# Kernel optimization log

Hardware: AMD Instinct MI355X
Metric: run time of the kernel (lower is better)

Reference implementation:

```python
import jax, jax.numpy as jnp
import numpy as np

EPS = 1e-5


def _layernorm(h, g, b):
    mu = jnp.mean(h, axis=-1, keepdims=True)
    var = jnp.mean((h - mu) ** 2, axis=-1, keepdims=True)
    return (h - mu) * jax.lax.rsqrt(var + EPS) * g + b


def _encode(x, W1, b1, g1, be1):
    # Linear -> LayerNorm -> ReLU (Dropout is identity in eval mode)
    h = x @ W1 + b1
    return jax.nn.relu(_layernorm(h, g1, be1))


def setup_inputs() -> dict:
    key = jax.random.key(0)
    ks = jax.random.split(key, 12)
    B, N, F, H, O = 131072, 8, 9, 64, 64

    def xavier(k, shape, gain=0.5):
        fan_in, fan_out = shape[0], shape[1]
        a = gain * np.sqrt(6.0 / (fan_in + fan_out))
        return jax.random.uniform(k, shape, jnp.float32, -a, a)

    return {
        "current_node_features": jax.random.normal(ks[0], (B, F), jnp.float32),
        "neighbor_features": jax.random.normal(ks[1], (B, N, F), jnp.float32),
        "neighbor_mask": jax.random.randint(ks[2], (B, N), 0, 2, jnp.int32),
        # node_encoder
        "W_enc": xavier(ks[3], (F, H)), "b_enc": jnp.zeros((H,), jnp.float32),
        "g_enc": jnp.ones((H,), jnp.float32), "be_enc": jnp.zeros((H,), jnp.float32),
        # attention MLP
        "W_a1": xavier(ks[4], (2 * H, H)), "b_a1": jnp.zeros((H,), jnp.float32),
        "W_a2": xavier(ks[5], (H, 1)), "b_a2": jnp.zeros((1,), jnp.float32),
        # output projection
        "W_out": xavier(ks[6], (2 * H, O)), "b_out": jnp.zeros((O,), jnp.float32),
        "g_out": jnp.ones((O,), jnp.float32), "be_out": jnp.zeros((O,), jnp.float32),
    }


def reference(current_node_features, neighbor_features, neighbor_mask,
              W_enc, b_enc, g_enc, be_enc,
              W_a1, b_a1, W_a2, b_a2,
              W_out, b_out, g_out, be_out):
    B, N = neighbor_mask.shape
    cur = _encode(current_node_features, W_enc, b_enc, g_enc, be_enc)      # [B, H]
    nbr = _encode(neighbor_features, W_enc, b_enc, g_enc, be_enc)          # [B, N, H]

    cur_exp = jnp.broadcast_to(cur[:, None, :], nbr.shape)                 # [B, N, H]
    att_in = jnp.concatenate([cur_exp, nbr], axis=-1)                      # [B, N, 2H]
    scores = (jax.nn.relu(att_in @ W_a1 + b_a1) @ W_a2 + b_a2)[..., 0]     # [B, N]
    scores = jnp.where(neighbor_mask == 0, -jnp.inf, scores)
    weights = jax.nn.softmax(scores, axis=-1)
    weights = jnp.where(jnp.isnan(weights), 0.0, weights)                  # all-masked rows -> 0

    aggregated = jnp.einsum("bn,bnh->bh", weights, nbr)                    # [B, H]
    combined = jnp.concatenate([cur, aggregated], axis=-1)                 # [B, 2H]
    out = jax.nn.relu(_layernorm(combined @ W_out + b_out, g_out, be_out)) # [B, O]
    return out
```

## Files before the change

kernel.cpp:

```cpp
#include <hip/hip_runtime.h>
#include <hip/hip_bf16.h>
#include <hip/hip_fp16.h>

typedef __attribute__((ext_vector_type(8))) short bf16x8;
typedef __attribute__((ext_vector_type(4))) float f32x4;
typedef __attribute__((ext_vector_type(4))) unsigned int u32x4;
typedef __attribute__((ext_vector_type(2))) unsigned int u32x2;

#define MFMA_BF16(A,B,C) __builtin_amdgcn_mfma_f32_16x16x32_bf16((A),(B),(C),0,0,0)

static __device__ __forceinline__ unsigned int pkbf2(float a, float b) {
  __hip_bfloat162 h = __float22bfloat162_rn(make_float2(a, b));
  unsigned int u; __builtin_memcpy(&u, &h, sizeof(u));
  return u;
}
static __device__ __forceinline__ unsigned short f2bf1(float f) {
  __hip_bfloat16 h = __float2bfloat16(f);
  unsigned short u; __builtin_memcpy(&u, &h, sizeof(u));
  return u;
}
static __device__ __forceinline__ int swz8(int v) { return (v ^ (v >> 3)) & 7; }

__global__ void gcn_prep(const float* __restrict__ wa1, const float* __restrict__ wout,
                         const float* __restrict__ wenc,
                         unsigned short* __restrict__ wa1f, unsigned short* __restrict__ woutf,
                         unsigned short* __restrict__ wencT) {
  int i = blockIdx.x * 512 + threadIdx.x;
  if (i < 8192) {
    int e = i & 7, l = (i >> 3) & 63, f = i >> 9;
    int kt = f >> 2, nt = f & 3;
    int k = 32 * kt + 8 * (l >> 4) + e;
    int col = 16 * nt + (l & 15);
    wa1f[i]  = f2bf1(wa1 [k * 64 + col]);
    woutf[i] = f2bf1(wout[k * 64 + col]);
  }
  int j = i - 8192;
  if (j >= 0 && j < 2048) {
    int e = j & 7, l = (j >> 3) & 63, mt = j >> 9;
    int k = 8 * (l >> 4) + e;
    int ch = 16 * mt + (l & 15);
    wencT[j] = (k < 9) ? f2bf1(wenc[k * 64 + ch]) : (unsigned short)0;
  }
}

__global__ __launch_bounds__(128, 4) void gcn_main(
    const float* __restrict__ xcur, const float* __restrict__ xnbr,
    const int*   __restrict__ msk,
    const float* __restrict__ benc, const float* __restrict__ genc, const float* __restrict__ beenc,
    const float* __restrict__ ba1,  const float* __restrict__ wa2,
    const float* __restrict__ bout, const float* __restrict__ gout, const float* __restrict__ beout,
    const unsigned short* __restrict__ wa1f, const unsigned short* __restrict__ woutf,
    const unsigned short* __restrict__ wencT,
    float* __restrict__ out) {

  __shared__ __align__(16) char smem[20992];
  unsigned short* sE   = (unsigned short*)smem;
  unsigned short* sAgg = (unsigned short*)(smem + 18432);
  float*          sS   = (float*)(smem + 20480);
  float*          sLN  = (float*)(smem + 20480);

  const int tid  = threadIdx.x;
  const int w    = tid >> 6;
  const int lane = tid & 63;
  const int lm   = lane & 15, g = lane >> 4;
  const int blk  = blockIdx.x;

  bf16x8 wf[16];
  bf16x8 wof[8];
  float bov[2], gvo[2], bevo[2];
  int4 mkv[4];

  {
    bf16x8 ef[4];
    #pragma unroll
    for (int mt = 0; mt < 4; mt++) ef[mt] = *(const bf16x8*)(wencT + (mt * 64 + lane) * 8);
    f32x4 bv[4], gv[4], bev[4];
    #pragma unroll
    for (int mt = 0; mt < 4; mt++) {
      bv[mt]  = *(const f32x4*)(benc  + 16 * mt + 4 * g);
      gv[mt]  = *(const f32x4*)(genc  + 16 * mt + 4 * g);
      bev[mt] = *(const f32x4*)(beenc + 16 * mt + 4 * g);
    }
    float nx[8];
    {
      const float* xb = (w < 8) ? (xnbr + ((size_t)blk * 128 + w * 16 + lm) * 9)
                                : (xcur + ((size_t)blk * 16 + lm) * 9);
      #pragma unroll
      for (int e = 0; e < 8; e++) nx[e] = 0.f;
      if (g == 0) {
        #pragma unroll
        for (int e = 0; e < 8; e++) nx[e] = xb[e];
      } else if (g == 1) nx[0] = xb[8];
    }
    #pragma unroll
    for (int s5 = 0; s5 < 5; s5++) {
      int t = 2 * s5 + w;
      if (t > 8) break;
      float xv[8];
      #pragma unroll
      for (int e = 0; e < 8; e++) xv[e] = nx[e];
      int tn = t + 2;
      if (tn <= 8) {
        const float* xb = (tn < 8) ? (xnbr + ((size_t)blk * 128 + tn * 16 + lm) * 9)
                                   : (xcur + ((size_t)blk * 16 + lm) * 9);
        #pragma unroll
        for (int e = 0; e < 8; e++) nx[e] = 0.f;
        if (g == 0) {
          #pragma unroll
          for (int e = 0; e < 8; e++) nx[e] = xb[e];
        } else if (g == 1) nx[0] = xb[8];
      }
      int v = (t < 8) ? (t * 16 + lm) : (128 + lm);
      u32x4 bq;
      #pragma unroll
      for (int e2 = 0; e2 < 4; e2++) bq[e2] = pkbf2(xv[2 * e2], xv[2 * e2 + 1]);
      bf16x8 bfr = __builtin_bit_cast(bf16x8, bq);
      f32x4 acc[4];
      #pragma unroll
      for (int mt = 0; mt < 4; mt++) acc[mt] = f32x4{0.f, 0.f, 0.f, 0.f};
      #pragma unroll
      for (int mt = 0; mt < 4; mt++) acc[mt] = MFMA_BF16(ef[mt], bfr, acc[mt]);
      float hv[16]; float s1 = 0.f, s2 = 0.f;
      #pragma unroll
      for (int mt = 0; mt < 4; mt++)
        #pragma unroll
        for (int i = 0; i < 4; i++) {
          float h = acc[mt][i] + bv[mt][i];
          hv[4 * mt + i] = h; s1 += h; s2 = fmaf(h, h, s2);
        }
      s1 += __shfl_xor(s1, 16); s1 += __shfl_xor(s1, 32);
      s2 += __shfl_xor(s2, 16); s2 += __shfl_xor(s2, 32);
      float mu = s1 * (1.f / 64.f);
      float rs = rsqrtf(s2 * (1.f / 64.f) - mu * mu + 1e-5f);
      int h8 = swz8(v);
      #pragma unroll
      for (int mt = 0; mt < 4; mt++) {
        float y0 = fmaxf(fmaf((hv[4 * mt + 0] - mu) * rs, gv[mt][0], bev[mt][0]), 0.f);
        float y1 = fmaxf(fmaf((hv[4 * mt + 1] - mu) * rs, gv[mt][1], bev[mt][1]), 0.f);
        float y2 = fmaxf(fmaf((hv[4 * mt + 2] - mu) * rs, gv[mt][2], bev[mt][2]), 0.f);
        float y3 = fmaxf(fmaf((hv[4 * mt + 3] - mu) * rs, gv[mt][3], bev[mt][3]), 0.f);
        int unit = (2 * mt + (g >> 1)) ^ h8;
        *(u32x2*)&sE[v * 64 + unit * 8 + ((g & 1) << 2)] = u32x2{pkbf2(y0, y1), pkbf2(y2, y3)};
      }
    }
    #pragma unroll
    for (int f = 0; f < 16; f++) wf[f] = *(const bf16x8*)(wa1f + (f * 64 + lane) * 8);
    #pragma unroll
    for (int mm = 0; mm < 4; mm++) {
      int r2 = 8 * w + 2 * mm + (g >> 1);
      mkv[mm] = *(const int4*)(msk + ((size_t)(blk * 16 + r2)) * 8 + 4 * (g & 1));
    }
  }
  __syncthreads();

  {
    float wa2v[4], ba1v[4];
    #pragma unroll
    for (int nt = 0; nt < 4; nt++) { wa2v[nt] = wa2[16 * nt + lm]; ba1v[nt] = ba1[16 * nt + lm]; }
    #pragma unroll
    for (int mm = 0; mm < 4; mm++) {
      int m = 4 * w + mm;
      int vb = 16 * m + lm,  hb = swz8(vb);
      int vcu = 128 + 2 * m + (lm >> 3), hcu = swz8(vcu);
      f32x4 a2[4];
      #pragma unroll
      for (int nt = 0; nt < 4; nt++) a2[nt] = f32x4{0.f, 0.f, 0.f, 0.f};
      #pragma unroll
      for (int ks = 0; ks < 2; ks++) {
        bf16x8 a = *(const bf16x8*)&sE[vcu * 64 + (((4 * ks + g) ^ hcu) << 3)];
        #pragma unroll
        for (int nt = 0; nt < 4; nt++) a2[nt] = MFMA_BF16(a, wf[ks * 4 + nt], a2[nt]);
      }
      #pragma unroll
      for (int ks = 0; ks < 2; ks++) {
        bf16x8 a = *(const bf16x8*)&sE[vb * 64 + (((4 * ks + g) ^ hb) << 3)];
        #pragma unroll
        for (int nt = 0; nt < 4; nt++) a2[nt] = MFMA_BF16(a, wf[(2 + ks) * 4 + nt], a2[nt]);
      }
      float p[4];
      #pragma unroll
      for (int i = 0; i < 4; i++) {
        float acc = 0.f;
        #pragma unroll
        for (int nt = 0; nt < 4; nt++)
          acc = fmaf(fmaxf(a2[nt][i] + ba1v[nt], 0.f), wa2v[nt], acc);
        acc += __shfl_xor(acc, 1); acc += __shfl_xor(acc, 2);
        acc += __shfl_xor(acc, 4); acc += __shfl_xor(acc, 8);
        p[i] = acc;
      }
      const int4 mk = mkv[mm];
      float sc0 = mk.x ? p[0] : -1e30f, sc1 = mk.y ? p[1] : -1e30f;
      float sc2 = mk.z ? p[2] : -1e30f, sc3 = mk.w ? p[3] : -1e30f;
      float mloc = fmaxf(fmaxf(sc0, sc1), fmaxf(sc2, sc3));
      float mx = fmaxf(mloc, __shfl_xor(mloc, 16));
      float e0 = mk.x ? __expf(sc0 - mx) : 0.f;
      float e1 = mk.y ? __expf(sc1 - mx) : 0.f;
      float e2 = mk.z ? __expf(sc2 - mx) : 0.f;
      float e3 = mk.w ? __expf(sc3 - mx) : 0.f;
      float ss = (e0 + e1) + (e2 + e3);
      ss += __shfl_xor(ss, 16);
      float rinv = (ss > 0.f) ? (1.f / ss) : 0.f;
      int r2 = 8 * w + 2 * mm + (g >> 1);
      if (lm == 0)
        *(float4*)&sS[r2 * 8 + 4 * (g & 1)] = make_float4(e0 * rinv, e1 * rinv, e2 * rinv, e3 * rinv);
    }
    const int nt0 = 2 * w;
    #pragma unroll
    for (int kt = 0; kt < 4; kt++)
      #pragma unroll
      for (int j = 0; j < 2; j++)
        wof[kt * 2 + j] = *(const bf16x8*)(woutf + ((kt * 4 + nt0 + j) * 64 + lane) * 8);
    #pragma unroll
    for (int j = 0; j < 2; j++) {
      bov[j]  = bout [16 * (nt0 + j) + lm];
      gvo[j]  = gout [16 * (nt0 + j) + lm];
      bevo[j] = beout[16 * (nt0 + j) + lm];
    }
  }
  __syncthreads();

  {
    int r = tid >> 3, cu = tid & 7;
    float4 wA = *(const float4*)&sS[r * 8];
    float4 wB = *(const float4*)&sS[r * 8 + 4];
    float wv[8] = {wA.x, wA.y, wA.z, wA.w, wB.x, wB.y, wB.z, wB.w};
    float a[8];
    #pragma unroll
    for (int e = 0; e < 8; e++) a[e] = 0.f;
    #pragma unroll
    for (int n = 0; n < 8; n++) {
      int v = 8 * r + n;
      u32x4 ev = *(const u32x4*)&sE[v * 64 + ((cu ^ swz8(v)) << 3)];
      float wn = wv[n];
      #pragma unroll
      for (int e2 = 0; e2 < 4; e2++) {
        unsigned int u = ev[e2];
        float lo = __builtin_bit_cast(float, u << 16);
        float hi = __builtin_bit_cast(float, u & 0xffff0000u);
        a[2 * e2]     = fmaf(wn, lo, a[2 * e2]);
        a[2 * e2 + 1] = fmaf(wn, hi, a[2 * e2 + 1]);
      }
    }
    *(u32x4*)&sAgg[r * 64 + ((cu ^ swz8(r)) << 3)] =
        u32x4{pkbf2(a[0], a[1]), pkbf2(a[2], a[3]), pkbf2(a[4], a[5]), pkbf2(a[6], a[7])};
  }
  __syncthreads();

  {
    const int nt0 = 2 * w;
    f32x4 acc[2];
    #pragma unroll
    for (int j = 0; j < 2; j++) acc[j] = f32x4{0.f, 0.f, 0.f, 0.f};
    const int vc = 128 + lm, hc = swz8(128 + lm);
    #pragma unroll
    for (int ks = 0; ks < 2; ks++) {
      bf16x8 a = *(const bf16x8*)&sE[vc * 64 + (((4 * ks + g) ^ hc) << 3)];
      #pragma unroll
      for (int j = 0; j < 2; j++) acc[j] = MFMA_BF16(a, wof[ks * 2 + j], acc[j]);
    }
    const int hA = swz8(lm);
    #pragma unroll
    for (int ks = 0; ks < 2; ks++) {
      bf16x8 a = *(const bf16x8*)&sAgg[lm * 64 + (((4 * ks + g) ^ hA) << 3)];
      #pragma unroll
      for (int j = 0; j < 2; j++) acc[j] = MFMA_BF16(a, wof[(2 + ks) * 2 + j], acc[j]);
    }
    float vl[2][4];
    #pragma unroll
    for (int j = 0; j < 2; j++)
      #pragma unroll
      for (int i = 0; i < 4; i++) vl[j][i] = acc[j][i] + bov[j];
    float s1[4], s2[4];
    #pragma unroll
    for (int i = 0; i < 4; i++) {
      s1[i] = vl[0][i] + vl[1][i];
      s2[i] = fmaf(vl[0][i], vl[0][i], vl[1][i] * vl[1][i]);
      s1[i] += __shfl_xor(s1[i], 1); s1[i] += __shfl_xor(s1[i], 2);
      s1[i] += __shfl_xor(s1[i], 4); s1[i] += __shfl_xor(s1[i], 8);
      s2[i] += __shfl_xor(s2[i], 1); s2[i] += __shfl_xor(s2[i], 2);
      s2[i] += __shfl_xor(s2[i], 4); s2[i] += __shfl_xor(s2[i], 8);
    }
    if (lm == 0) {
      #pragma unroll
      for (int i = 0; i < 4; i++)
        *(float2*)&sLN[(4 * g + i) * 4 + 2 * w] = make_float2(s1[i], s2[i]);
    }
    __syncthreads();
    #pragma unroll
    for (int i = 0; i < 4; i++) {
      float2 pa = *(const float2*)&sLN[(4 * g + i) * 4];
      float2 pb = *(const float2*)&sLN[(4 * g + i) * 4 + 2];
      float S1 = pa.x + pb.x, S2 = pa.y + pb.y;
      float mu = S1 * (1.f / 64.f);
      float rs = rsqrtf(S2 * (1.f / 64.f) - mu * mu + 1e-5f);
      size_t orow = (size_t)blk * 16 + 4 * g + i;
      #pragma unroll
      for (int j = 0; j < 2; j++) {
        float y = fmaxf(fmaf((vl[j][i] - mu) * rs, gvo[j], bevo[j]), 0.f);
        out[orow * 64 + 16 * (nt0 + j) + lm] = y;
      }
    }
  }
}

extern "C" void kernel_launch(void* const* d_in, const int* in_sizes, int n_in,
                              void* d_out, int out_size, void* d_ws, size_t ws_size,
                              hipStream_t stream) {
  const float* xcur = (const float*)d_in[0];
  const float* xnbr = (const float*)d_in[1];
  const int*   msk  = (const int*)  d_in[2];
  const float* wenc = (const float*)d_in[3];
  const float* benc = (const float*)d_in[4];
  const float* genc = (const float*)d_in[5];
  const float* bee  = (const float*)d_in[6];
  const float* wa1  = (const float*)d_in[7];
  const float* ba1  = (const float*)d_in[8];
  const float* wa2  = (const float*)d_in[9];
  const float* wout = (const float*)d_in[11];
  const float* bo   = (const float*)d_in[12];
  const float* go   = (const float*)d_in[13];
  const float* beo  = (const float*)d_in[14];

  unsigned short* wa1f  = (unsigned short*)d_ws;
  unsigned short* woutf = (unsigned short*)((char*)d_ws + 16384);
  unsigned short* wencT = (unsigned short*)((char*)d_ws + 32768);

  gcn_prep<<<20, 512, 0, stream>>>(wa1, wout, wenc, wa1f, woutf, wencT);
  gcn_main<<<8192, 128, 0, stream>>>(xcur, xnbr, msk, benc, genc, bee, ba1, wa2,
                                     bo, go, beo, wa1f, woutf, wencT, (float*)d_out);
}
```

Measured before the change: 74.77 us.

## Use single-wave blocks of 8 nodes to drop barriers and use DPP reductions

Each block becomes one 64-lane wave that handles 8 nodes instead of 16, so every __syncthreads disappears and LDS use shrinks, which should allow more resident blocks. Biases are folded into the MFMA accumulator initial values, and the 16-lane reductions use DPP row rotations in place of shuffles. The price is that half the lanes do redundant work on the current-node encode and in the output MFMA, the output weights are loaded by every wave, and twice as many blocks are launched.

```diff
diff --git a/kernel.cpp b/kernel.cpp
--- a/kernel.cpp
+++ b/kernel.cpp
@@ -20,6 +20,19 @@
   return u;
 }
 static __device__ __forceinline__ int swz8(int v) { return (v ^ (v >> 3)) & 7; }
+
+template<int N>
+static __device__ __forceinline__ float rot16(float x) {
+  return __builtin_bit_cast(float,
+      __builtin_amdgcn_mov_dpp(__builtin_bit_cast(int, x), 0x120 + N, 0xF, 0xF, false));
+}
+static __device__ __forceinline__ float sum16(float x) {
+  x += rot16<8>(x);
+  x += rot16<4>(x);
+  x += rot16<2>(x);
+  x += rot16<1>(x);
+  return x;
+}
 
 __global__ void gcn_prep(const float* __restrict__ wa1, const float* __restrict__ wout,
                          const float* __restrict__ wenc,
@@ -43,7 +56,7 @@
   }
 }
 
-__global__ __launch_bounds__(128, 4) void gcn_main(
+__global__ __launch_bounds__(64, 4) void gcn_main(
     const float* __restrict__ xcur, const float* __restrict__ xnbr,
     const int*   __restrict__ msk,
     const float* __restrict__ benc, const float* __restrict__ genc, const float* __restrict__ beenc,
@@ -53,22 +66,20 @@
     const unsigned short* __restrict__ wencT,
     float* __restrict__ out) {
 
-  __shared__ __align__(16) char smem[20992];
+  __shared__ __align__(16) char smem[9472];
   unsigned short* sE   = (unsigned short*)smem;
-  unsigned short* sAgg = (unsigned short*)(smem + 18432);
-  float*          sS   = (float*)(smem + 20480);
-  float*          sLN  = (float*)(smem + 20480);
-
-  const int tid  = threadIdx.x;
-  const int w    = tid >> 6;
-  const int lane = tid & 63;
-  const int lm   = lane & 15, g = lane >> 4;
-  const int blk  = blockIdx.x;
+  unsigned short* sAgg = (unsigned short*)smem;
+  float*          sS   = (float*)(smem + 9216);
+
+  const int lane = threadIdx.x;
+  const int lm = lane & 15, g = lane >> 4;
+  const int blk = blockIdx.x;
 
   bf16x8 wf[16];
-  bf16x8 wof[8];
-  float bov[2], gvo[2], bevo[2];
+  bf16x8 wofc[8];
   int4 mkv[4];
+  float wa2v[4], ba1v[4];
+  float bovv[4], gvo[4], bevo[4];
 
   {
     bf16x8 ef[4];
@@ -83,8 +94,7 @@
     }
     float nx[8];
     {
-      const float* xb = (w < 8) ? (xnbr + ((size_t)blk * 128 + w * 16 + lm) * 9)
-                                : (xcur + ((size_t)blk * 16 + lm) * 9);
+      const float* xb = xnbr + ((size_t)blk * 64 + lm) * 9;
       #pragma unroll
       for (int e = 0; e < 8; e++) nx[e] = 0.f;
       if (g == 0) {
@@ -93,16 +103,13 @@
       } else if (g == 1) nx[0] = xb[8];
     }
     #pragma unroll
-    for (int s5 = 0; s5 < 5; s5++) {
-      int t = 2 * s5 + w;
-      if (t > 8) break;
+    for (int t = 0; t < 5; t++) {
       float xv[8];
       #pragma unroll
       for (int e = 0; e < 8; e++) xv[e] = nx[e];
-      int tn = t + 2;
-      if (tn <= 8) {
-        const float* xb = (tn < 8) ? (xnbr + ((size_t)blk * 128 + tn * 16 + lm) * 9)
-                                   : (xcur + ((size_t)blk * 16 + lm) * 9);
+      if (t < 4) {
+        const float* xb = (t < 3) ? (xnbr + ((size_t)blk * 64 + (t + 1) * 16 + lm) * 9)
+                                  : (xcur + ((size_t)blk * 8 + (lm & 7)) * 9);
         #pragma unroll
         for (int e = 0; e < 8; e++) nx[e] = 0.f;
         if (g == 0) {
@@ -110,61 +117,58 @@
           for (int e = 0; e < 8; e++) nx[e] = xb[e];
         } else if (g == 1) nx[0] = xb[8];
       }
-      int v = (t < 8) ? (t * 16 + lm) : (128 + lm);
       u32x4 bq;
       #pragma unroll
       for (int e2 = 0; e2 < 4; e2++) bq[e2] = pkbf2(xv[2 * e2], xv[2 * e2 + 1]);
       bf16x8 bfr = __builtin_bit_cast(bf16x8, bq);
       f32x4 acc[4];
       #pragma unroll
-      for (int mt = 0; mt < 4; mt++) acc[mt] = f32x4{0.f, 0.f, 0.f, 0.f};
+      for (int mt = 0; mt < 4; mt++) acc[mt] = bv[mt];
       #pragma unroll
       for (int mt = 0; mt < 4; mt++) acc[mt] = MFMA_BF16(ef[mt], bfr, acc[mt]);
-      float hv[16]; float s1 = 0.f, s2 = 0.f;
+      float s1 = 0.f, s2 = 0.f;
       #pragma unroll
       for (int mt = 0; mt < 4; mt++)
         #pragma unroll
-        for (int i = 0; i < 4; i++) {
-          float h = acc[mt][i] + bv[mt][i];
-          hv[4 * mt + i] = h; s1 += h; s2 = fmaf(h, h, s2);
-        }
+        for (int i = 0; i < 4; i++) { float h = acc[mt][i]; s1 += h; s2 = fmaf(h, h, s2); }
       s1 += __shfl_xor(s1, 16); s1 += __shfl_xor(s1, 32);
       s2 += __shfl_xor(s2, 16); s2 += __shfl_xor(s2, 32);
       float mu = s1 * (1.f / 64.f);
       float rs = rsqrtf(s2 * (1.f / 64.f) - mu * mu + 1e-5f);
+      int v = (t < 4) ? (t * 16 + lm) : (64 + lm);
       int h8 = swz8(v);
-      #pragma unroll
-      for (int mt = 0; mt < 4; mt++) {
-        float y0 = fmaxf(fmaf((hv[4 * mt + 0] - mu) * rs, gv[mt][0], bev[mt][0]), 0.f);
-        float y1 = fmaxf(fmaf((hv[4 * mt + 1] - mu) * rs, gv[mt][1], bev[mt][1]), 0.f);
-        float y2 = fmaxf(fmaf((hv[4 * mt + 2] - mu) * rs, gv[mt][2], bev[mt][2]), 0.f);
-        float y3 = fmaxf(fmaf((hv[4 * mt + 3] - mu) * rs, gv[mt][3], bev[mt][3]), 0.f);
-        int unit = (2 * mt + (g >> 1)) ^ h8;
-        *(u32x2*)&sE[v * 64 + unit * 8 + ((g & 1) << 2)] = u32x2{pkbf2(y0, y1), pkbf2(y2, y3)};
+      if (t < 4 || lm < 8) {
+        #pragma unroll
+        for (int mt = 0; mt < 4; mt++) {
+          float y0 = fmaxf(fmaf((acc[mt][0] - mu) * rs, gv[mt][0], bev[mt][0]), 0.f);
+          float y1 = fmaxf(fmaf((acc[mt][1] - mu) * rs, gv[mt][1], bev[mt][1]), 0.f);
+          float y2 = fmaxf(fmaf((acc[mt][2] - mu) * rs, gv[mt][2], bev[mt][2]), 0.f);
+          float y3 = fmaxf(fmaf((acc[mt][3] - mu) * rs, gv[mt][3], bev[mt][3]), 0.f);
+          int unit = (2 * mt + (g >> 1)) ^ h8;
+          *(u32x2*)&sE[v * 64 + unit * 8 + ((g & 1) << 2)] = u32x2{pkbf2(y0, y1), pkbf2(y2, y3)};
+        }
       }
     }
     #pragma unroll
     for (int f = 0; f < 16; f++) wf[f] = *(const bf16x8*)(wa1f + (f * 64 + lane) * 8);
     #pragma unroll
     for (int mm = 0; mm < 4; mm++) {
-      int r2 = 8 * w + 2 * mm + (g >> 1);
-      mkv[mm] = *(const int4*)(msk + ((size_t)(blk * 16 + r2)) * 8 + 4 * (g & 1));
-    }
-  }
-  __syncthreads();
+      int r2 = 2 * mm + (g >> 1);
+      mkv[mm] = *(const int4*)(msk + ((size_t)(blk * 8 + r2)) * 8 + 4 * (g & 1));
+    }
+    #pragma unroll
+    for (int nt = 0; nt < 4; nt++) { wa2v[nt] = wa2[16 * nt + lm]; ba1v[nt] = ba1[16 * nt + lm]; }
+  }
 
   {
-    float wa2v[4], ba1v[4];
-    #pragma unroll
-    for (int nt = 0; nt < 4; nt++) { wa2v[nt] = wa2[16 * nt + lm]; ba1v[nt] = ba1[16 * nt + lm]; }
     #pragma unroll
     for (int mm = 0; mm < 4; mm++) {
-      int m = 4 * w + mm;
-      int vb = 16 * m + lm,  hb = swz8(vb);
-      int vcu = 128 + 2 * m + (lm >> 3), hcu = swz8(vcu);
+      int vb = 16 * mm + lm,  hb = swz8(vb);
+      int vcu = 64 + 2 * mm + (lm >> 3), hcu = swz8(vcu);
       f32x4 a2[4];
       #pragma unroll
-      for (int nt = 0; nt < 4; nt++) a2[nt] = f32x4{0.f, 0.f, 0.f, 0.f};
+      for (int nt = 0; nt < 4; nt++)
+        a2[nt] = f32x4{ba1v[nt], ba1v[nt], ba1v[nt], ba1v[nt]};
       #pragma unroll
       for (int ks = 0; ks < 2; ks++) {
         bf16x8 a = *(const bf16x8*)&sE[vcu * 64 + (((4 * ks + g) ^ hcu) << 3)];
@@ -183,10 +187,8 @@
         float acc = 0.f;
         #pragma unroll
         for (int nt = 0; nt < 4; nt++)
-          acc = fmaf(fmaxf(a2[nt][i] + ba1v[nt], 0.f), wa2v[nt], acc);
-        acc += __shfl_xor(acc, 1); acc += __shfl_xor(acc, 2);
-        acc += __shfl_xor(acc, 4); acc += __shfl_xor(acc, 8);
-        p[i] = acc;
+          acc = fmaf(fmaxf(a2[nt][i], 0.f), wa2v[nt], acc);
+        p[i] = sum16(acc);
       }
       const int4 mk = mkv[mm];
       float sc0 = mk.x ? p[0] : -1e30f, sc1 = mk.y ? p[1] : -1e30f;
@@ -200,27 +202,25 @@
       float ss = (e0 + e1) + (e2 + e3);
       ss += __shfl_xor(ss, 16);
       float rinv = (ss > 0.f) ? (1.f / ss) : 0.f;
-      int r2 = 8 * w + 2 * mm + (g >> 1);
+      int r2 = 2 * mm + (g >> 1);
       if (lm == 0)
         *(float4*)&sS[r2 * 8 + 4 * (g & 1)] = make_float4(e0 * rinv, e1 * rinv, e2 * rinv, e3 * rinv);
     }
-    const int nt0 = 2 * w;
-    #pragma unroll
-    for (int kt = 0; kt < 4; kt++)
-      #pragma unroll
-      for (int j = 0; j < 2; j++)
-        wof[kt * 2 + j] = *(const bf16x8*)(woutf + ((kt * 4 + nt0 + j) * 64 + lane) * 8);
-    #pragma unroll
-    for (int j = 0; j < 2; j++) {
-      bov[j]  = bout [16 * (nt0 + j) + lm];
-      gvo[j]  = gout [16 * (nt0 + j) + lm];
-      bevo[j] = beout[16 * (nt0 + j) + lm];
-    }
-  }
-  __syncthreads();
-
+    #pragma unroll
+    for (int f = 0; f < 8; f++) wofc[f] = *(const bf16x8*)(woutf + (f * 64 + lane) * 8);
+    #pragma unroll
+    for (int nt = 0; nt < 4; nt++) {
+      bovv[nt] = bout [16 * nt + lm];
+      gvo[nt]  = gout [16 * nt + lm];
+      bevo[nt] = beout[16 * nt + lm];
+    }
+  }
+
+  bf16x8 wofa[8];
   {
-    int r = tid >> 3, cu = tid & 7;
+    #pragma unroll
+    for (int f = 0; f < 8; f++) wofa[f] = *(const bf16x8*)(woutf + ((8 + f) * 64 + lane) * 8);
+    int r = lane >> 3, cu = lane & 7;
     float4 wA = *(const float4*)&sS[r * 8];
     float4 wB = *(const float4*)&sS[r * 8 + 4];
     float wv[8] = {wA.x, wA.y, wA.z, wA.w, wB.x, wB.y, wB.z, wB.w};
@@ -244,60 +244,46 @@
     *(u32x4*)&sAgg[r * 64 + ((cu ^ swz8(r)) << 3)] =
         u32x4{pkbf2(a[0], a[1]), pkbf2(a[2], a[3]), pkbf2(a[4], a[5]), pkbf2(a[6], a[7])};
   }
-  __syncthreads();
 
   {
-    const int nt0 = 2 * w;
-    f32x4 acc[2];
-    #pragma unroll
-    for (int j = 0; j < 2; j++) acc[j] = f32x4{0.f, 0.f, 0.f, 0.f};
-    const int vc = 128 + lm, hc = swz8(128 + lm);
+    f32x4 acc[4];
+    #pragma unroll
+    for (int nt = 0; nt < 4; nt++)
+      acc[nt] = f32x4{bovv[nt], bovv[nt], bovv[nt], bovv[nt]};
+    const int vc = 64 + (lm & 7), hc = swz8(vc);
     #pragma unroll
     for (int ks = 0; ks < 2; ks++) {
       bf16x8 a = *(const bf16x8*)&sE[vc * 64 + (((4 * ks + g) ^ hc) << 3)];
       #pragma unroll
-      for (int j = 0; j < 2; j++) acc[j] = MFMA_BF16(a, wof[ks * 2 + j], acc[j]);
-    }
-    const int hA = swz8(lm);
+      for (int nt = 0; nt < 4; nt++) acc[nt] = MFMA_BF16(a, wofc[ks * 4 + nt], acc[nt]);
+    }
+    const int ra = lm & 7, hA = swz8(ra);
     #pragma unroll
     for (int ks = 0; ks < 2; ks++) {
-      bf16x8 a = *(const bf16x8*)&sAgg[lm * 64 + (((4 * ks + g) ^ hA) << 3)];
-      #pragma unroll
-      for (int j = 0; j < 2; j++) acc[j] = MFMA_BF16(a, wof[(2 + ks) * 2 + j], acc[j]);
-    }
-    float vl[2][4];
-    #pragma unroll
-    for (int j = 0; j < 2; j++)
-      #pragma unroll
-      for (int i = 0; i < 4; i++) vl[j][i] = acc[j][i] + bov[j];
+      bf16x8 a = *(const bf16x8*)&sAgg[ra * 64 + (((4 * ks + g) ^ hA) << 3)];
+      #pragma unroll
+      for (int nt = 0; nt < 4; nt++) acc[nt] = MFMA_BF16(a, wofa[ks * 4 + nt], acc[nt]);
+    }
     float s1[4], s2[4];
     #pragma unroll
     for (int i = 0; i < 4; i++) {
-      s1[i] = vl[0][i] + vl[1][i];
-      s2[i] = fmaf(vl[0][i], vl[0][i], vl[1][i] * vl[1][i]);
-      s1[i] += __shfl_xor(s1[i], 1); s1[i] += __shfl_xor(s1[i], 2);
-      s1[i] += __shfl_xor(s1[i], 4); s1[i] += __shfl_xor(s1[i], 8);
-      s2[i] += __shfl_xor(s2[i], 1); s2[i] += __shfl_xor(s2[i], 2);
-      s2[i] += __shfl_xor(s2[i], 4); s2[i] += __shfl_xor(s2[i], 8);
-    }
-    if (lm == 0) {
-      #pragma unroll
-      for (int i = 0; i < 4; i++)
-        *(float2*)&sLN[(4 * g + i) * 4 + 2 * w] = make_float2(s1[i], s2[i]);
-    }
-    __syncthreads();
-    #pragma unroll
-    for (int i = 0; i < 4; i++) {
-      float2 pa = *(const float2*)&sLN[(4 * g + i) * 4];
-      float2 pb = *(const float2*)&sLN[(4 * g + i) * 4 + 2];
-      float S1 = pa.x + pb.x, S2 = pa.y + pb.y;
-      float mu = S1 * (1.f / 64.f);
-      float rs = rsqrtf(S2 * (1.f / 64.f) - mu * mu + 1e-5f);
-      size_t orow = (size_t)blk * 16 + 4 * g + i;
-      #pragma unroll
-      for (int j = 0; j < 2; j++) {
-        float y = fmaxf(fmaf((vl[j][i] - mu) * rs, gvo[j], bevo[j]), 0.f);
-        out[orow * 64 + 16 * (nt0 + j) + lm] = y;
+      s1[i] = (acc[0][i] + acc[1][i]) + (acc[2][i] + acc[3][i]);
+      s2[i] = fmaf(acc[0][i], acc[0][i], acc[1][i] * acc[1][i])
+            + fmaf(acc[2][i], acc[2][i], acc[3][i] * acc[3][i]);
+      s1[i] = sum16(s1[i]);
+      s2[i] = sum16(s2[i]);
+    }
+    if (g < 2) {
+      #pragma unroll
+      for (int i = 0; i < 4; i++) {
+        float mu = s1[i] * (1.f / 64.f);
+        float rs = rsqrtf(s2[i] * (1.f / 64.f) - mu * mu + 1e-5f);
+        size_t orow = (size_t)blk * 8 + 4 * g + i;
+        #pragma unroll
+        for (int nt = 0; nt < 4; nt++) {
+          float y = fmaxf(fmaf((acc[nt][i] - mu) * rs, gvo[nt], bevo[nt]), 0.f);
+          out[orow * 64 + 16 * nt + lm] = y;
+        }
       }
     }
   }
@@ -326,6 +312,6 @@
   unsigned short* wencT = (unsigned short*)((char*)d_ws + 32768);
 
   gcn_prep<<<20, 512, 0, stream>>>(wa1, wout, wenc, wa1f, woutf, wencT);
-  gcn_main<<<8192, 128, 0, stream>>>(xcur, xnbr, msk, benc, genc, bee, ba1, wa2,
+  gcn_main<<<16384, 64, 0, stream>>>(xcur, xnbr, msk, benc, genc, bee, ba1, wa2,
                                      bo, go, beo, wa1f, woutf, wencT, (float*)d_out);
 }
```

After: 78.52 us. 5.0% more time.
